# Kernel optimization log

Hardware: AMD Instinct MI355X
Metric: run time of the kernel (lower is better)

The kernel has to match this reference:

```python
import jax, jax.numpy as jnp
import numpy as np

GROUPS = 8
EPS = 1e-5
NUM_HEADS = 8


def group_norm(x, gamma, beta):
    # x: [B, C, N]; GroupNorm over (C//G, N) per group, per sample (torch semantics)
    B, C, N = x.shape
    xg = x.reshape(B, GROUPS, (C // GROUPS) * N)
    mean = xg.mean(axis=-1, keepdims=True)
    var = xg.var(axis=-1, keepdims=True)
    xn = ((xg - mean) * jax.lax.rsqrt(var + EPS)).reshape(B, C, N)
    return xn * gamma[None, :, None] + beta[None, :, None]


def setup_inputs() -> dict:
    key = jax.random.key(0)
    ks = jax.random.split(key, 6)
    B, N, C = 4, 2048, 512
    s = 0.02
    return {
        "x": jax.random.normal(ks[0], (B, N, C), jnp.float32),
        "pe": jax.random.normal(ks[1], (B, N, C), jnp.float32),
        "qkv_w": jax.random.normal(ks[2], (3 * C, C), jnp.float32) * s,
        "proj_w": jax.random.normal(ks[3], (C, C), jnp.float32) * s,
        "proj_b": jnp.zeros((C,), jnp.float32),
        "conv1_w": jax.random.normal(ks[4], (C, C), jnp.float32) * s,
        "conv1_b": jnp.zeros((C,), jnp.float32),
        "gn1_g": jnp.ones((C,), jnp.float32),
        "gn1_b": jnp.zeros((C,), jnp.float32),
        "conv2_w": jax.random.normal(ks[5], (C, C), jnp.float32) * s,
        "conv2_b": jnp.zeros((C,), jnp.float32),
        "gn2_g": jnp.ones((C,), jnp.float32),
        "gn2_b": jnp.zeros((C,), jnp.float32),
    }


def reference(x, pe, qkv_w, proj_w, proj_b, conv1_w, conv1_b, gn1_g, gn1_b,
              conv2_w, conv2_b, gn2_g, gn2_b):
    B, N, C = x.shape
    H = NUM_HEADS
    D = C // H
    scale = D ** -0.5

    pe_t = pe.transpose(0, 2, 1)  # [B, C, N]
    # Conv1d(kernel=1) == per-position linear over channels
    p1 = group_norm(jnp.einsum('oc,bcn->bon', conv1_w, pe_t) + conv1_b[None, :, None], gn1_g, gn1_b)
    p2 = group_norm(jnp.einsum('oc,bcn->bon', conv2_w, pe_t) + conv2_b[None, :, None], gn2_g, gn2_b)
    pe_1 = p1.transpose(0, 2, 1)                 # [B, N, C]
    pe_attn = jax.nn.sigmoid(jnp.einsum('bnc,bcm->bnm', pe_1, p2))  # [B, N, N]

    qkv = (x @ qkv_w.T).reshape(B, N, 3, H, D).transpose(2, 0, 3, 1, 4)  # [3, B, H, N, D]
    q, k, v = qkv[0], qkv[1], qkv[2]

    attn = jnp.einsum('bhnd,bhmd->bhnm', q, k) * scale
    attn = attn * pe_attn[:, None, :, :]
    attn = jax.nn.softmax(attn, axis=-1)

    out = jnp.einsum('bhnm,bhmd->bhnd', attn, v)          # [B, H, N, D]
    out = out.transpose(0, 2, 1, 3).reshape(B, N, C)
    return out @ proj_w.T + proj_b
```

## Files before the change

kernel.cpp:

```cpp
#include <hip/hip_runtime.h>
#include <hip/hip_bf16.h>

typedef __attribute__((ext_vector_type(8))) short bf16x8;
typedef __attribute__((ext_vector_type(4))) float f32x4;

__device__ __forceinline__ float bfu2f(unsigned int u) {
    return __uint_as_float(u << 16);
}
__device__ __forceinline__ unsigned short f2bfu(float f) {
    unsigned int u = __float_as_uint(f);
    u += 0x7fffu + ((u >> 16) & 1u);
    return (unsigned short)(u >> 16);
}

__global__ __launch_bounds__(256) void cvt_all(
    const float* __restrict__ x, unsigned short* __restrict__ xb,
    const float* __restrict__ pe, unsigned short* __restrict__ peb,
    const float* __restrict__ w0, unsigned short* __restrict__ d0,
    const float* __restrict__ w1, unsigned short* __restrict__ d1,
    const float* __restrict__ w2, unsigned short* __restrict__ d2,
    const float* __restrict__ w3, unsigned short* __restrict__ d3,
    const float* __restrict__ c1bias, const float* __restrict__ c2bias,
    float* __restrict__ biasws) {
    const int tid = threadIdx.x;
    if (blockIdx.x == 0) {
        if (tid < 128) ((float4*)biasws)[tid] = ((const float4*)c1bias)[tid];
        else ((float4*)biasws)[tid] = ((const float4*)c2bias)[tid - 128];
    }
    int i = blockIdx.x * 256 + tid;
    const int stride = gridDim.x * 256;
    for (; i < 1441792; i += stride) {
        if (i < 1048576) {
            float4 v = reinterpret_cast<const float4*>(x)[i];
            ushort4 o;
            o.x = f2bfu(v.x); o.y = f2bfu(v.y); o.z = f2bfu(v.z); o.w = f2bfu(v.w);
            reinterpret_cast<ushort4*>(xb)[i] = o;
            float4 u = reinterpret_cast<const float4*>(pe)[i];
            ushort4 p;
            p.x = f2bfu(u.x); p.y = f2bfu(u.y); p.z = f2bfu(u.z); p.w = f2bfu(u.w);
            reinterpret_cast<ushort4*>(peb)[i] = p;
        } else {
            int j = i - 1048576;
            const float* s; unsigned short* d;
            if (j < 196608)      { s = w0; d = d0; }
            else if (j < 262144) { s = w1; d = d1; j -= 196608; }
            else if (j < 327680) { s = w2; d = d2; j -= 262144; }
            else                 { s = w3; d = d3; j -= 327680; }
            float4 v = reinterpret_cast<const float4*>(s)[j];
            ushort4 o;
            o.x = f2bfu(v.x); o.y = f2bfu(v.y); o.z = f2bfu(v.z); o.w = f2bfu(v.w);
            reinterpret_cast<ushort4*>(d)[j] = o;
        }
    }
}

template <int EPI>
__global__ __launch_bounds__(256) void gemm_nt(
    const unsigned short* __restrict__ A, const unsigned short* __restrict__ B,
    void* __restrict__ C0, void* __restrict__ C1, void* __restrict__ C2,
    const float* __restrict__ bias, int K, long sA, long sB, long sC,
    int nx, int ny) {
    __shared__ unsigned short As[2][128 * 32];
    __shared__ unsigned short Bs[2][128 * 32];
    int lin = blockIdx.x;
    const int qsw = gridDim.x >> 3;
    lin = (lin & 7) * qsw + (lin >> 3);
    const int bx = lin % nx;
    const int t2 = lin / nx;
    const int by = t2 % ny;
    const int bz = t2 / ny;
    const int tid = threadIdx.x;
    const int l = tid & 63, w = tid >> 6;
    const int wr = w >> 1, wc = w & 1, lr = l & 15, lh = l >> 4;
    const int m0 = by * 128, n0 = bx * 128;
    A += (size_t)bz * sA;
    B += (size_t)bz * sB;
    f32x4 acc[4][4] = {};

    const int srow = l >> 2, sslot = l & 3;
    auto stage = [&](int bufi, int k0) {
#pragma unroll
        for (int i = 0; i < 2; i++) {
            const int row = w * 32 + i * 16 + srow;
            const int cs = (sslot ^ (row & 3)) * 8;
            const int ldsoff = (w * 32 + i * 16) * 32;
            __builtin_amdgcn_global_load_lds(
                (const __attribute__((address_space(1))) void*)(A + (size_t)(m0 + row) * K + k0 + cs),
                (__attribute__((address_space(3))) void*)&As[bufi][ldsoff], 16, 0, 0);
            __builtin_amdgcn_global_load_lds(
                (const __attribute__((address_space(1))) void*)(B + (size_t)(n0 + row) * K + k0 + cs),
                (__attribute__((address_space(3))) void*)&Bs[bufi][ldsoff], 16, 0, 0);
        }
    };

    const int nks = K >> 5;
    stage(0, 0);
    asm volatile("s_waitcnt vmcnt(0)" ::: "memory");
    __builtin_amdgcn_s_barrier();
    __builtin_amdgcn_sched_barrier(0);

    const int colA = (lh ^ (lr & 3)) << 3;
    for (int ks = 0; ks < nks; ks++) {
        const int cur = ks & 1;
        if (ks + 1 < nks) stage(cur ^ 1, (ks + 1) << 5);
        bf16x8 af[4], bfr[4];
#pragma unroll
        for (int i = 0; i < 4; i++)
            af[i] = *reinterpret_cast<const bf16x8*>(&As[cur][(wr * 64 + i * 16 + lr) * 32 + colA]);
#pragma unroll
        for (int i = 0; i < 4; i++)
            bfr[i] = *reinterpret_cast<const bf16x8*>(&Bs[cur][(wc * 64 + i * 16 + lr) * 32 + colA]);
        __builtin_amdgcn_s_setprio(1);
#pragma unroll
        for (int mi = 0; mi < 4; mi++)
#pragma unroll
            for (int ni = 0; ni < 4; ni++)
                acc[mi][ni] = __builtin_amdgcn_mfma_f32_16x16x32_bf16(af[mi], bfr[ni], acc[mi][ni], 0, 0, 0);
        __builtin_amdgcn_s_setprio(0);
        if (ks + 1 < nks) {
            asm volatile("s_waitcnt vmcnt(0) lgkmcnt(0)" ::: "memory");
            __builtin_amdgcn_s_barrier();
            __builtin_amdgcn_sched_barrier(0);
        }
    }

    float sgn = 0.f, qgn = 0.f;
#pragma unroll
    for (int mi = 0; mi < 4; mi++) {
#pragma unroll
        for (int ni = 0; ni < 4; ni++) {
#pragma unroll
            for (int r = 0; r < 4; r++) {
                const int row = m0 + wr * 64 + mi * 16 + lh * 4 + r;
                const int col = n0 + wc * 64 + ni * 16 + lr;
                float v = acc[mi][ni][r];
                if constexpr (EPI == 0) {
                    v += bias[bz * 512 + col];
                    sgn += v; qgn += v * v;
                    ((unsigned short*)C0)[(size_t)bz * sC + (size_t)row * 512 + col] = f2bfu(v);
                } else if constexpr (EPI == 1) {
                    const int part = col >> 9, hh = (col >> 6) & 7, d = col & 63;
                    const int b = row >> 11, n = row & 2047;
                    const size_t bh = (size_t)(b * 8 + hh);
                    if (part == 0)
                        ((unsigned short*)C0)[(bh * 2048 + n) * 64 + d] = f2bfu(v * 0.1803368801111244f);
                    else if (part == 1)
                        ((unsigned short*)C1)[(bh * 2048 + n) * 64 + d] = f2bfu(v);
                    else
                        ((unsigned short*)C2)[(bh * 64 + d) * 2048 + n] = f2bfu(v);
                } else if constexpr (EPI == 2) {
                    const float sg = 1.0f / (1.0f + __expf(-v));
                    ((unsigned short*)C0)[(size_t)bz * sC + (size_t)row * 2048 + col] = f2bfu(sg);
                } else {
                    ((float*)C0)[(size_t)row * 512 + col] = v + bias[col];
                }
            }
        }
    }
    if constexpr (EPI == 0) {
#pragma unroll
        for (int s = 1; s < 64; s <<= 1) {
            sgn += __shfl_xor(sgn, s);
            qgn += __shfl_xor(qgn, s);
        }
        if (l == 0) {
            const int bg = ((by >> 4) << 3) + bx * 2 + wc;
            float* part = (float*)C1;
            atomicAdd(&part[(bz * 32 + bg) * 2 + 0], sgn);
            atomicAdd(&part[(bz * 32 + bg) * 2 + 1], qgn);
        }
    }
}

__global__ __launch_bounds__(256) void gn_apply(unsigned short* __restrict__ c1,
                                                unsigned short* __restrict__ c2,
                                                const float* __restrict__ part,
                                                const float* __restrict__ g1, const float* __restrict__ b1,
                                                const float* __restrict__ g2, const float* __restrict__ b2) {
    __shared__ float sst[2][32][2];
    const int tid = threadIdx.x;
    if (tid < 64) {
        const int z = tid >> 5, bg = tid & 31;
        const float S = part[(z * 32 + bg) * 2 + 0];
        const float Q = part[(z * 32 + bg) * 2 + 1];
        const float inv = 1.0f / 131072.0f;
        const float m = S * inv;
        const float v = fmaxf(Q * inv - m * m, 0.f);
        sst[z][bg][0] = m;
        sst[z][bg][1] = rsqrtf(v + 1e-5f);
    }
    __syncthreads();
    int i = blockIdx.x * 256 + tid;
    const int stride = gridDim.x * 256;
    for (; i < 524288; i += stride) {
        const size_t e = (size_t)i * 8;
        const int b = (int)(e >> 20);
        const int o = (int)(e & 511);
        const int g = o >> 6;
        const int bg = (b << 3) + g;
        const float m1 = sst[0][bg][0], r1 = sst[0][bg][1];
        const float m2 = sst[1][bg][0], r2 = sst[1][bg][1];
        uint4 v1 = *reinterpret_cast<const uint4*>(c1 + e);
        uint4 v2 = *reinterpret_cast<const uint4*>(c2 + e);
        unsigned int a1[4] = {v1.x, v1.y, v1.z, v1.w};
        unsigned int a2[4] = {v2.x, v2.y, v2.z, v2.w};
        unsigned int o1[4], o2[4];
#pragma unroll
        for (int j = 0; j < 4; j++) {
            const int oo = o + j * 2;
            float x0 = (bfu2f(a1[j] & 0xffffu) - m1) * r1 * g1[oo] + b1[oo];
            float x1 = (bfu2f(a1[j] >> 16) - m1) * r1 * g1[oo + 1] + b1[oo + 1];
            o1[j] = (unsigned int)f2bfu(x0) | ((unsigned int)f2bfu(x1) << 16);
            float y0 = (bfu2f(a2[j] & 0xffffu) - m2) * r2 * g2[oo] + b2[oo];
            float y1 = (bfu2f(a2[j] >> 16) - m2) * r2 * g2[oo + 1] + b2[oo + 1];
            o2[j] = (unsigned int)f2bfu(y0) | ((unsigned int)f2bfu(y1) << 16);
        }
        uint4 w1; w1.x = o1[0]; w1.y = o1[1]; w1.z = o1[2]; w1.w = o1[3];
        uint4 w2; w2.x = o2[0]; w2.y = o2[1]; w2.z = o2[2]; w2.w = o2[3];
        *reinterpret_cast<uint4*>(c1 + e) = w1;
        *reinterpret_cast<uint4*>(c2 + e) = w2;
    }
}

__global__ __launch_bounds__(256, 4) void attn_fused(
    const unsigned short* __restrict__ qb, const unsigned short* __restrict__ kb,
    const unsigned short* __restrict__ vT, const unsigned short* __restrict__ pea,
    unsigned short* __restrict__ hbuf) {
    __shared__ unsigned short Ks[2][64 * 64];
    __shared__ unsigned short Vs[2][64 * 64];
    __shared__ unsigned short Pl[4][16 * 64];
    const int tid = threadIdx.x, l = tid & 63, w = tid >> 6;
    const int lr = l & 15, lh = l >> 4;
    const int bid = blockIdx.x;
    const int h = bid >> 7, rst = bid & 127, nt = rst & 31, b = rst >> 5;
    const size_t bh = (size_t)(b * 8 + h);
    const unsigned short* qp = qb + bh * 2048 * 64;
    const unsigned short* kp = kb + bh * 2048 * 64;
    const unsigned short* vp = vT + bh * 64 * 2048;
    const unsigned short* pep = pea + (size_t)b * 2048 * 2048;
    const int n0 = nt * 64;

    bf16x8 qf[2];
    qf[0] = *reinterpret_cast<const bf16x8*>(qp + (size_t)(n0 + 16 * w + lr) * 64 + lh * 8);
    qf[1] = *reinterpret_cast<const bf16x8*>(qp + (size_t)(n0 + 16 * w + lr) * 64 + 32 + lh * 8);

    const int swz = (lr & 7) << 4;
    const int colK0 = ((16 * lh) ^ swz) >> 1;
    const int colK1 = ((64 + 16 * lh) ^ swz) >> 1;

    const unsigned short* perp = pep + (size_t)(n0 + 16 * w + lr) * 2048;
    uint2 peR[4];
#pragma unroll
    for (int mf = 0; mf < 4; mf++)
        peR[mf] = *reinterpret_cast<const uint2*>(perp + 16 * mf + 4 * lh);

    f32x4 oacc[4] = {};
    float mrun = -1e30f, lrun = 0.f;

    const int srow = l >> 3, sslot = l & 7;
    auto stage_kv = [&](int bufi, int m0) {
#pragma unroll
        for (int i = 0; i < 2; i++) {
            const int row = w * 16 + i * 8 + srow;
            const int cs = (sslot ^ (row & 7)) * 8;
            const int ldsoff = (w * 16 + i * 8) * 64;
            __builtin_amdgcn_global_load_lds(
                (const __attribute__((address_space(1))) void*)(kp + (size_t)(m0 + row) * 64 + cs),
                (__attribute__((address_space(3))) void*)&Ks[bufi][ldsoff], 16, 0, 0);
            __builtin_amdgcn_global_load_lds(
                (const __attribute__((address_space(1))) void*)(vp + (size_t)row * 2048 + m0 + cs),
                (__attribute__((address_space(3))) void*)&Vs[bufi][ldsoff], 16, 0, 0);
        }
    };

    stage_kv(0, 0);
    asm volatile("s_waitcnt vmcnt(0)" ::: "memory");
    __builtin_amdgcn_s_barrier();
    __builtin_amdgcn_sched_barrier(0);

    for (int mt = 0; mt < 32; mt++) {
        const int cur = mt & 1;
        if (mt + 1 < 32) stage_kv(cur ^ 1, (mt + 1) * 64);
        const unsigned short* Kb = Ks[cur];
        const unsigned short* Vb = Vs[cur];

        f32x4 st[4] = {};
        __builtin_amdgcn_s_setprio(1);
#pragma unroll
        for (int mf = 0; mf < 4; mf++) {
            bf16x8 kf0 = *reinterpret_cast<const bf16x8*>(&Kb[(mf * 16 + lr) * 64 + colK0]);
            bf16x8 kf1 = *reinterpret_cast<const bf16x8*>(&Kb[(mf * 16 + lr) * 64 + colK1]);
            st[mf] = __builtin_amdgcn_mfma_f32_16x16x32_bf16(kf0, qf[0], st[mf], 0, 0, 0);
            st[mf] = __builtin_amdgcn_mfma_f32_16x16x32_bf16(kf1, qf[1], st[mf], 0, 0, 0);
        }
        __builtin_amdgcn_s_setprio(0);

        float p[4][4];
#pragma unroll
        for (int mf = 0; mf < 4; mf++) {
            p[mf][0] = st[mf][0] * bfu2f(peR[mf].x & 0xffffu);
            p[mf][1] = st[mf][1] * bfu2f(peR[mf].x >> 16);
            p[mf][2] = st[mf][2] * bfu2f(peR[mf].y & 0xffffu);
            p[mf][3] = st[mf][3] * bfu2f(peR[mf].y >> 16);
        }
        uint2 peN[4];
        if (mt + 1 < 32) {
            const unsigned short* pn = perp + (mt + 1) * 64;
#pragma unroll
            for (int mf = 0; mf < 4; mf++)
                peN[mf] = *reinterpret_cast<const uint2*>(pn + 16 * mf + 4 * lh);
        }
        float pm = fmaxf(p[0][0], p[0][1]);
        pm = fmaxf(fmaxf(pm, p[0][2]), p[0][3]);
#pragma unroll
        for (int mf = 1; mf < 4; mf++) {
            pm = fmaxf(fmaxf(pm, p[mf][0]), p[mf][1]);
            pm = fmaxf(fmaxf(pm, p[mf][2]), p[mf][3]);
        }
        pm = fmaxf(pm, __shfl_xor(pm, 16));
        pm = fmaxf(pm, __shfl_xor(pm, 32));
        if (__any(pm > mrun + 11.5416f)) {
            const float mnew = fmaxf(mrun, pm);
            const float fac = __builtin_amdgcn_exp2f(mrun - mnew);
            lrun *= fac;
#pragma unroll
            for (int df = 0; df < 4; df++)
#pragma unroll
                for (int r = 0; r < 4; r++) oacc[df][r] *= fac;
            mrun = mnew;
        }
        float ss = 0.f;
        unsigned int pk[8];
#pragma unroll
        for (int mf = 0; mf < 4; mf++) {
#pragma unroll
            for (int t = 0; t < 2; t++) {
                const float a = __builtin_amdgcn_exp2f(p[mf][2 * t] - mrun);
                const float c = __builtin_amdgcn_exp2f(p[mf][2 * t + 1] - mrun);
                unsigned int pkv;
                asm("v_cvt_pk_bf16_f32 %0, %1, %2" : "=v"(pkv) : "v"(a), "v"(c));
                pk[mf * 2 + t] = pkv;
                ss += a + c;
            }
        }
        ss += __shfl_xor(ss, 16);
        ss += __shfl_xor(ss, 32);
        lrun += ss;
        unsigned short* PlW = Pl[w];
        const int plswz = (lr & 7) << 4;
#pragma unroll
        for (int mf = 0; mf < 4; mf++)
#pragma unroll
            for (int t = 0; t < 2; t++) {
                const int cb = (mf * 32 + lh * 8 + 4 * t) ^ plswz;
                *reinterpret_cast<unsigned int*>(&PlW[lr * 64 + (cb >> 1)]) = pk[mf * 2 + t];
            }
        bf16x8 pb0 = *reinterpret_cast<const bf16x8*>(&PlW[lr * 64 + (((lh * 16) ^ plswz) >> 1)]);
        bf16x8 pb1 = *reinterpret_cast<const bf16x8*>(&PlW[lr * 64 + (((64 + lh * 16) ^ plswz) >> 1)]);
        __builtin_amdgcn_s_setprio(1);
#pragma unroll
        for (int df = 0; df < 4; df++) {
            bf16x8 vf0 = *reinterpret_cast<const bf16x8*>(&Vb[(df * 16 + lr) * 64 + colK0]);
            bf16x8 vf1 = *reinterpret_cast<const bf16x8*>(&Vb[(df * 16 + lr) * 64 + colK1]);
            oacc[df] = __builtin_amdgcn_mfma_f32_16x16x32_bf16(vf0, pb0, oacc[df], 0, 0, 0);
            oacc[df] = __builtin_amdgcn_mfma_f32_16x16x32_bf16(vf1, pb1, oacc[df], 0, 0, 0);
        }
        __builtin_amdgcn_s_setprio(0);
        if (mt + 1 < 32) {
            asm volatile("s_waitcnt vmcnt(0) lgkmcnt(0)" ::: "memory");
            __builtin_amdgcn_s_barrier();
            __builtin_amdgcn_sched_barrier(0);
#pragma unroll
            for (int mf = 0; mf < 4; mf++) peR[mf] = peN[mf];
        }
    }
    const float inv = 1.0f / lrun;
    const size_t base = ((size_t)b * 2048 + n0 + 16 * w + lr) * 512 + h * 64;
#pragma unroll
    for (int df = 0; df < 4; df++) {
#pragma unroll
        for (int t = 0; t < 2; t++) {
            const unsigned int ua = f2bfu(oacc[df][2 * t] * inv);
            const unsigned int uc = f2bfu(oacc[df][2 * t + 1] * inv);
            *reinterpret_cast<unsigned int*>(&hbuf[base + 16 * df + 4 * lh + 2 * t]) = ua | (uc << 16);
        }
    }
}

extern "C" void kernel_launch(void* const* d_in, const int* in_sizes, int n_in,
                              void* d_out, int out_size, void* d_ws, size_t ws_size,
                              hipStream_t stream) {
    const float* x       = (const float*)d_in[0];
    const float* pe      = (const float*)d_in[1];
    const float* qkv_w   = (const float*)d_in[2];
    const float* proj_w  = (const float*)d_in[3];
    const float* proj_b  = (const float*)d_in[4];
    const float* conv1_w = (const float*)d_in[5];
    const float* conv1_b = (const float*)d_in[6];
    const float* gn1_g   = (const float*)d_in[7];
    const float* gn1_b   = (const float*)d_in[8];
    const float* conv2_w = (const float*)d_in[9];
    const float* conv2_b = (const float*)d_in[10];
    const float* gn2_g   = (const float*)d_in[11];
    const float* gn2_b   = (const float*)d_in[12];
    float* out = (float*)d_out;

    char* ws = (char*)d_ws;
    size_t off = 0;
    auto alloc = [&](size_t bytes) -> void* {
        void* p = ws + off;
        off += (bytes + 255) & ~(size_t)255;
        return p;
    };
    unsigned short* xb     = (unsigned short*)alloc(8388608);
    unsigned short* peb    = (unsigned short*)alloc(8388608);
    unsigned short* qkvwb  = (unsigned short*)alloc(1572864);
    unsigned short* projwb = (unsigned short*)alloc(524288);
    unsigned short* w1b    = (unsigned short*)alloc(524288);
    unsigned short* w2b    = (unsigned short*)alloc(524288);
    unsigned short* c1b    = (unsigned short*)alloc(8388608);
    unsigned short* c2b    = (unsigned short*)alloc(8388608);
    unsigned short* qbuf   = (unsigned short*)alloc(8388608);
    unsigned short* kbuf   = (unsigned short*)alloc(8388608);
    unsigned short* vtb    = (unsigned short*)alloc(8388608);
    unsigned short* peatt  = (unsigned short*)alloc(33554432);
    unsigned short* hbuf   = (unsigned short*)alloc(8388608);
    float* part            = (float*)alloc(512);
    float* biasws          = (float*)alloc(4096);

    dim3 blk(256);
    hipMemsetAsync(part, 0, 512, stream);
    cvt_all<<<2048, blk, 0, stream>>>(x, xb, pe, peb, qkv_w, qkvwb, proj_w, projwb,
                                      conv1_w, w1b, conv2_w, w2b, conv1_b, conv2_b, biasws);

    gemm_nt<0><<<dim3(512), blk, 0, stream>>>(peb, w1b, c1b, part, nullptr, biasws,
                                              512, 0, 262144, 4194304, 4, 64);
    gn_apply<<<1024, blk, 0, stream>>>(c1b, c2b, part, gn1_g, gn1_b, gn2_g, gn2_b);
    gemm_nt<1><<<dim3(768), blk, 0, stream>>>(xb, qkvwb, qbuf, kbuf, vtb, nullptr,
                                              512, 0, 0, 0, 12, 64);
    gemm_nt<2><<<dim3(1024), blk, 0, stream>>>(c1b, c2b, peatt, nullptr, nullptr, nullptr,
                                               512, 1048576, 1048576, 4194304, 16, 16);
    attn_fused<<<dim3(1024), blk, 0, stream>>>(qbuf, kbuf, vtb, peatt, hbuf);
    gemm_nt<3><<<dim3(256), blk, 0, stream>>>(hbuf, projwb, out, nullptr, nullptr, proj_b,
                                              512, 0, 0, 0, 4, 64);
}
```

Measured before the change: 226.3 us.

## Merge conv and QKV GEMMs into one launch; widen attention blocks to 512 threads

Combines the conv1/conv2 projection GEMM and the QKV projection GEMM into a single kernel that branches on block index, so the two independent GEMMs share one launch and fill the GPU together. The attention kernel now runs 8 waves per block (128 query rows) instead of 4, which halves the K/V tile loads per query row and halves the grid. The risks are more LDS and register pressure per block, which could lower occupancy, and a heterogeneous grid whose two halves have different epilogues.

```diff
diff --git a/kernel.cpp b/kernel.cpp
--- a/kernel.cpp
+++ b/kernel.cpp
@@ -54,12 +54,133 @@
     }
 }
 
+__global__ __launch_bounds__(256) void gemm_cq(
+    const unsigned short* __restrict__ peb, const unsigned short* __restrict__ wcb,
+    unsigned short* __restrict__ c1b, float* __restrict__ part, const float* __restrict__ biasws,
+    const unsigned short* __restrict__ xb, const unsigned short* __restrict__ qkvwb,
+    unsigned short* __restrict__ qbuf, unsigned short* __restrict__ kbuf,
+    unsigned short* __restrict__ vtb) {
+    __shared__ unsigned short As[2][128 * 32];
+    __shared__ unsigned short Bs[2][128 * 32];
+    const int bid = blockIdx.x;
+    const bool isconv = bid < 512;
+    int bx, by, bz;
+    const unsigned short* A;
+    const unsigned short* B;
+    if (isconv) {
+        int lin = ((bid & 7) << 6) + (bid >> 3);
+        bx = lin & 3; by = (lin >> 2) & 63; bz = lin >> 8;
+        A = peb; B = wcb + (size_t)bz * 262144;
+    } else {
+        int l2 = bid - 512;
+        int lin = (l2 & 7) * 96 + (l2 >> 3);
+        bx = lin % 12; by = lin / 12; bz = 0;
+        A = xb; B = qkvwb;
+    }
+    const int tid = threadIdx.x;
+    const int l = tid & 63, w = tid >> 6;
+    const int wr = w >> 1, wc = w & 1, lr = l & 15, lh = l >> 4;
+    const int m0 = by * 128, n0 = bx * 128;
+    f32x4 acc[4][4] = {};
+
+    const int srow = l >> 2, sslot = l & 3;
+    auto stage = [&](int bufi, int k0) {
+#pragma unroll
+        for (int i = 0; i < 2; i++) {
+            const int row = w * 32 + i * 16 + srow;
+            const int cs = (sslot ^ (row & 3)) * 8;
+            const int ldsoff = (w * 32 + i * 16) * 32;
+            __builtin_amdgcn_global_load_lds(
+                (const __attribute__((address_space(1))) void*)(A + (size_t)(m0 + row) * 512 + k0 + cs),
+                (__attribute__((address_space(3))) void*)&As[bufi][ldsoff], 16, 0, 0);
+            __builtin_amdgcn_global_load_lds(
+                (const __attribute__((address_space(1))) void*)(B + (size_t)(n0 + row) * 512 + k0 + cs),
+                (__attribute__((address_space(3))) void*)&Bs[bufi][ldsoff], 16, 0, 0);
+        }
+    };
+
+    stage(0, 0);
+    asm volatile("s_waitcnt vmcnt(0)" ::: "memory");
+    __builtin_amdgcn_s_barrier();
+    __builtin_amdgcn_sched_barrier(0);
+
+    const int colA = (lh ^ (lr & 3)) << 3;
+    for (int ks = 0; ks < 16; ks++) {
+        const int cur = ks & 1;
+        if (ks + 1 < 16) stage(cur ^ 1, (ks + 1) << 5);
+        bf16x8 af[4], bfr[4];
+#pragma unroll
+        for (int i = 0; i < 4; i++)
+            af[i] = *reinterpret_cast<const bf16x8*>(&As[cur][(wr * 64 + i * 16 + lr) * 32 + colA]);
+#pragma unroll
+        for (int i = 0; i < 4; i++)
+            bfr[i] = *reinterpret_cast<const bf16x8*>(&Bs[cur][(wc * 64 + i * 16 + lr) * 32 + colA]);
+        __builtin_amdgcn_s_setprio(1);
+#pragma unroll
+        for (int mi = 0; mi < 4; mi++)
+#pragma unroll
+            for (int ni = 0; ni < 4; ni++)
+                acc[mi][ni] = __builtin_amdgcn_mfma_f32_16x16x32_bf16(af[mi], bfr[ni], acc[mi][ni], 0, 0, 0);
+        __builtin_amdgcn_s_setprio(0);
+        if (ks + 1 < 16) {
+            asm volatile("s_waitcnt vmcnt(0) lgkmcnt(0)" ::: "memory");
+            __builtin_amdgcn_s_barrier();
+            __builtin_amdgcn_sched_barrier(0);
+        }
+    }
+
+    if (isconv) {
+        float sgn = 0.f, qgn = 0.f;
+#pragma unroll
+        for (int mi = 0; mi < 4; mi++)
+#pragma unroll
+            for (int ni = 0; ni < 4; ni++)
+#pragma unroll
+                for (int r = 0; r < 4; r++) {
+                    const int row = m0 + wr * 64 + mi * 16 + lh * 4 + r;
+                    const int col = n0 + wc * 64 + ni * 16 + lr;
+                    float v = acc[mi][ni][r] + biasws[bz * 512 + col];
+                    sgn += v; qgn += v * v;
+                    c1b[(size_t)bz * 4194304 + (size_t)row * 512 + col] = f2bfu(v);
+                }
+#pragma unroll
+        for (int s = 1; s < 64; s <<= 1) {
+            sgn += __shfl_xor(sgn, s);
+            qgn += __shfl_xor(qgn, s);
+        }
+        if (l == 0) {
+            const int bg = ((by >> 4) << 3) + bx * 2 + wc;
+            atomicAdd(&part[(bz * 32 + bg) * 2 + 0], sgn);
+            atomicAdd(&part[(bz * 32 + bg) * 2 + 1], qgn);
+        }
+    } else {
+#pragma unroll
+        for (int mi = 0; mi < 4; mi++)
+#pragma unroll
+            for (int ni = 0; ni < 4; ni++)
+#pragma unroll
+                for (int r = 0; r < 4; r++) {
+                    const int row = m0 + wr * 64 + mi * 16 + lh * 4 + r;
+                    const int col = n0 + wc * 64 + ni * 16 + lr;
+                    const float v = acc[mi][ni][r];
+                    const int part_ = col >> 9, hh = (col >> 6) & 7, d = col & 63;
+                    const int b = row >> 11, n = row & 2047;
+                    const size_t bh = (size_t)(b * 8 + hh);
+                    if (part_ == 0)
+                        qbuf[(bh * 2048 + n) * 64 + d] = f2bfu(v * 0.1803368801111244f);
+                    else if (part_ == 1)
+                        kbuf[(bh * 2048 + n) * 64 + d] = f2bfu(v);
+                    else
+                        vtb[(bh * 64 + d) * 2048 + n] = f2bfu(v);
+                }
+    }
+}
+
 template <int EPI>
 __global__ __launch_bounds__(256) void gemm_nt(
     const unsigned short* __restrict__ A, const unsigned short* __restrict__ B,
-    void* __restrict__ C0, void* __restrict__ C1, void* __restrict__ C2,
-    const float* __restrict__ bias, int K, long sA, long sB, long sC,
-    int nx, int ny) {
+    void* __restrict__ C0, const float* __restrict__ bias,
+    int K, long sA, long sB, long sC, int nx, int ny) {
     __shared__ unsigned short As[2][128 * 32];
     __shared__ unsigned short Bs[2][128 * 32];
     int lin = blockIdx.x;
@@ -124,7 +245,6 @@
         }
     }
 
-    float sgn = 0.f, qgn = 0.f;
 #pragma unroll
     for (int mi = 0; mi < 4; mi++) {
 #pragma unroll
@@ -134,40 +254,13 @@
                 const int row = m0 + wr * 64 + mi * 16 + lh * 4 + r;
                 const int col = n0 + wc * 64 + ni * 16 + lr;
                 float v = acc[mi][ni][r];
-                if constexpr (EPI == 0) {
-                    v += bias[bz * 512 + col];
-                    sgn += v; qgn += v * v;
-                    ((unsigned short*)C0)[(size_t)bz * sC + (size_t)row * 512 + col] = f2bfu(v);
-                } else if constexpr (EPI == 1) {
-                    const int part = col >> 9, hh = (col >> 6) & 7, d = col & 63;
-                    const int b = row >> 11, n = row & 2047;
-                    const size_t bh = (size_t)(b * 8 + hh);
-                    if (part == 0)
-                        ((unsigned short*)C0)[(bh * 2048 + n) * 64 + d] = f2bfu(v * 0.1803368801111244f);
-                    else if (part == 1)
-                        ((unsigned short*)C1)[(bh * 2048 + n) * 64 + d] = f2bfu(v);
-                    else
-                        ((unsigned short*)C2)[(bh * 64 + d) * 2048 + n] = f2bfu(v);
-                } else if constexpr (EPI == 2) {
+                if constexpr (EPI == 2) {
                     const float sg = 1.0f / (1.0f + __expf(-v));
                     ((unsigned short*)C0)[(size_t)bz * sC + (size_t)row * 2048 + col] = f2bfu(sg);
                 } else {
                     ((float*)C0)[(size_t)row * 512 + col] = v + bias[col];
                 }
             }
-        }
-    }
-    if constexpr (EPI == 0) {
-#pragma unroll
-        for (int s = 1; s < 64; s <<= 1) {
-            sgn += __shfl_xor(sgn, s);
-            qgn += __shfl_xor(qgn, s);
-        }
-        if (l == 0) {
-            const int bg = ((by >> 4) << 3) + bx * 2 + wc;
-            float* part = (float*)C1;
-            atomicAdd(&part[(bz * 32 + bg) * 2 + 0], sgn);
-            atomicAdd(&part[(bz * 32 + bg) * 2 + 1], qgn);
         }
     }
 }
@@ -222,33 +315,33 @@
     }
 }
 
-__global__ __launch_bounds__(256, 4) void attn_fused(
+__global__ __launch_bounds__(512, 4) void attn_fused(
     const unsigned short* __restrict__ qb, const unsigned short* __restrict__ kb,
     const unsigned short* __restrict__ vT, const unsigned short* __restrict__ pea,
     unsigned short* __restrict__ hbuf) {
     __shared__ unsigned short Ks[2][64 * 64];
     __shared__ unsigned short Vs[2][64 * 64];
-    __shared__ unsigned short Pl[4][16 * 64];
+    __shared__ unsigned short Pl[8][16 * 64];
     const int tid = threadIdx.x, l = tid & 63, w = tid >> 6;
     const int lr = l & 15, lh = l >> 4;
     const int bid = blockIdx.x;
-    const int h = bid >> 7, rst = bid & 127, nt = rst & 31, b = rst >> 5;
+    const int h = bid >> 6, rst = bid & 63, nt = rst & 15, b = rst >> 4;
     const size_t bh = (size_t)(b * 8 + h);
     const unsigned short* qp = qb + bh * 2048 * 64;
     const unsigned short* kp = kb + bh * 2048 * 64;
     const unsigned short* vp = vT + bh * 64 * 2048;
     const unsigned short* pep = pea + (size_t)b * 2048 * 2048;
-    const int n0 = nt * 64;
+    const int qrow = nt * 128 + 16 * w + lr;
 
     bf16x8 qf[2];
-    qf[0] = *reinterpret_cast<const bf16x8*>(qp + (size_t)(n0 + 16 * w + lr) * 64 + lh * 8);
-    qf[1] = *reinterpret_cast<const bf16x8*>(qp + (size_t)(n0 + 16 * w + lr) * 64 + 32 + lh * 8);
+    qf[0] = *reinterpret_cast<const bf16x8*>(qp + (size_t)qrow * 64 + lh * 8);
+    qf[1] = *reinterpret_cast<const bf16x8*>(qp + (size_t)qrow * 64 + 32 + lh * 8);
 
     const int swz = (lr & 7) << 4;
     const int colK0 = ((16 * lh) ^ swz) >> 1;
     const int colK1 = ((64 + 16 * lh) ^ swz) >> 1;
 
-    const unsigned short* perp = pep + (size_t)(n0 + 16 * w + lr) * 2048;
+    const unsigned short* perp = pep + (size_t)qrow * 2048;
     uint2 peR[4];
 #pragma unroll
     for (int mf = 0; mf < 4; mf++)
@@ -259,18 +352,15 @@
 
     const int srow = l >> 3, sslot = l & 7;
     auto stage_kv = [&](int bufi, int m0) {
-#pragma unroll
-        for (int i = 0; i < 2; i++) {
-            const int row = w * 16 + i * 8 + srow;
-            const int cs = (sslot ^ (row & 7)) * 8;
-            const int ldsoff = (w * 16 + i * 8) * 64;
-            __builtin_amdgcn_global_load_lds(
-                (const __attribute__((address_space(1))) void*)(kp + (size_t)(m0 + row) * 64 + cs),
-                (__attribute__((address_space(3))) void*)&Ks[bufi][ldsoff], 16, 0, 0);
-            __builtin_amdgcn_global_load_lds(
-                (const __attribute__((address_space(1))) void*)(vp + (size_t)row * 2048 + m0 + cs),
-                (__attribute__((address_space(3))) void*)&Vs[bufi][ldsoff], 16, 0, 0);
-        }
+        const int row = w * 8 + srow;
+        const int cs = (sslot ^ srow) * 8;
+        const int ldsoff = w * 512;
+        __builtin_amdgcn_global_load_lds(
+            (const __attribute__((address_space(1))) void*)(kp + (size_t)(m0 + row) * 64 + cs),
+            (__attribute__((address_space(3))) void*)&Ks[bufi][ldsoff], 16, 0, 0);
+        __builtin_amdgcn_global_load_lds(
+            (const __attribute__((address_space(1))) void*)(vp + (size_t)row * 2048 + m0 + cs),
+            (__attribute__((address_space(3))) void*)&Vs[bufi][ldsoff], 16, 0, 0);
     };
 
     stage_kv(0, 0);
@@ -375,7 +465,7 @@
         }
     }
     const float inv = 1.0f / lrun;
-    const size_t base = ((size_t)b * 2048 + n0 + 16 * w + lr) * 512 + h * 64;
+    const size_t base = ((size_t)b * 2048 + qrow) * 512 + h * 64;
 #pragma unroll
     for (int df = 0; df < 4; df++) {
 #pragma unroll
@@ -433,14 +523,12 @@
     cvt_all<<<2048, blk, 0, stream>>>(x, xb, pe, peb, qkv_w, qkvwb, proj_w, projwb,
                                       conv1_w, w1b, conv2_w, w2b, conv1_b, conv2_b, biasws);
 
-    gemm_nt<0><<<dim3(512), blk, 0, stream>>>(peb, w1b, c1b, part, nullptr, biasws,
-                                              512, 0, 262144, 4194304, 4, 64);
+    gemm_cq<<<dim3(1280), blk, 0, stream>>>(peb, w1b, c1b, part, biasws,
+                                            xb, qkvwb, qbuf, kbuf, vtb);
     gn_apply<<<1024, blk, 0, stream>>>(c1b, c2b, part, gn1_g, gn1_b, gn2_g, gn2_b);
-    gemm_nt<1><<<dim3(768), blk, 0, stream>>>(xb, qkvwb, qbuf, kbuf, vtb, nullptr,
-                                              512, 0, 0, 0, 12, 64);
-    gemm_nt<2><<<dim3(1024), blk, 0, stream>>>(c1b, c2b, peatt, nullptr, nullptr, nullptr,
+    gemm_nt<2><<<dim3(1024), blk, 0, stream>>>(c1b, c2b, peatt, nullptr,
                                                512, 1048576, 1048576, 4194304, 16, 16);
-    attn_fused<<<dim3(1024), blk, 0, stream>>>(qbuf, kbuf, vtb, peatt, hbuf);
-    gemm_nt<3><<<dim3(256), blk, 0, stream>>>(hbuf, projwb, out, nullptr, nullptr, proj_b,
+    attn_fused<<<dim3(512), dim3(512), 0, stream>>>(qbuf, kbuf, vtb, peatt, hbuf);
+    gemm_nt<3><<<dim3(256), blk, 0, stream>>>(hbuf, projwb, out, proj_b,
                                               512, 0, 0, 0, 4, 64);
 }
```

After: 226.2 us. No clear change (-0.0%).
